# Kernel tuning notes

Measured on AMD Instinct MI355X. Metric: run time of the kernel, lower is better.

## Reference

```python
import jax, jax.numpy as jnp
import numpy as np

N_HEAD = 12
N_EMBD = 768


def setup_inputs() -> dict:
    key = jax.random.key(0)
    k1, k2, k3, k4, k5 = jax.random.split(key, 5)
    B, T, C = 4, 2048, N_EMBD
    s = 0.02
    x = jax.random.normal(k1, (B, T, C), dtype=jnp.float32)
    w_attn = jax.random.normal(k2, (C, 3 * C), dtype=jnp.float32) * s
    b_attn = jnp.zeros((3 * C,), dtype=jnp.float32)
    w_proj = jax.random.normal(k3, (C, C), dtype=jnp.float32) * s
    b_proj = jnp.zeros((C,), dtype=jnp.float32)
    return {"x": x, "w_attn": w_attn, "b_attn": b_attn, "w_proj": w_proj, "b_proj": b_proj}


def reference(x, w_attn, b_attn, w_proj, b_proj):
    # dropout omitted (eval mode / dropout=0.0)
    B, T, C = x.shape
    H = N_HEAD
    D = C // H  # head dim
    qkv = x @ w_attn + b_attn                      # [B,T,3C]
    q, k, v = jnp.split(qkv, 3, axis=-1)
    q = q.reshape(B, T, H, D).transpose(0, 2, 1, 3)  # [B,H,T,D]
    k = k.reshape(B, T, H, D).transpose(0, 2, 1, 3)
    v = v.reshape(B, T, H, D).transpose(0, 2, 1, 3)
    att = jnp.einsum('bhqd,bhkd->bhqk', q, k) * (1.0 / np.sqrt(D))  # [B,H,T,T]
    causal = jnp.tril(jnp.ones((T, T), dtype=bool))
    att = jnp.where(causal[None, None], att, -jnp.inf)
    att = jax.nn.softmax(att, axis=-1)
    y = jnp.einsum('bhqk,bhkd->bhqd', att, v)      # [B,H,T,D]
    y = y.transpose(0, 2, 1, 3).reshape(B, T, C)
    return y @ w_proj + b_proj
```

## Files before the change

kernel.cpp:

```cpp
#include <hip/hip_runtime.h>
#include <stdint.h>

typedef unsigned short ushort_t;

#define T_SEQ 2048
#define BATCH 4
#define NHEAD 12
#define CEMB 768
#define HDIM 64
#define C3 2304

__device__ __forceinline__ ushort_t f2b_hw(float f) {
  union { __bf16 h; ushort_t u; } p;
  p.h = (__bf16)f;
  return p.u;
}
__device__ __forceinline__ uint32_t pkbf16(float lo, float hi) {
  union { __bf16 h[2]; uint32_t u; } p;
  p.h[0] = (__bf16)lo; p.h[1] = (__bf16)hi;
  return p.u;
}

typedef __attribute__((address_space(3))) unsigned int lds_u32_t;
typedef const __attribute__((address_space(1))) unsigned int glb_u32_t;
__device__ __forceinline__ void async_cp16(const void* g, void* l) {
  __builtin_amdgcn_global_load_lds((glb_u32_t*)g, (lds_u32_t*)l, 16, 0, 0);
}

__global__ __launch_bounds__(256) void prep_k(const float* __restrict__ x, ushort_t* __restrict__ xb,
                                              const float* __restrict__ wa, ushort_t* __restrict__ wT,
                                              const float* __restrict__ wp, ushort_t* __restrict__ wpT) {
  const int blk = blockIdx.x;
  const int tid = threadIdx.x;
  if (blk < 3072) {
    const int i = blk * 256 + tid;
    float4 a = ((const float4*)x)[2 * i];
    float4 b = ((const float4*)x)[2 * i + 1];
    uint4 v;
    v.x = pkbf16(a.x, a.y); v.y = pkbf16(a.z, a.w);
    v.z = pkbf16(b.x, b.y); v.w = pkbf16(b.z, b.w);
    ((uint4*)xb)[i] = v;
    return;
  }
  __shared__ ushort_t tile[32][33];
  const float* in; ushort_t* out; int R, C, bx, by;
  if (blk < 4800) {
    const int t = blk - 3072;
    in = wa; out = wT; R = CEMB; C = C3;
    bx = t % 72; by = t / 72;
  } else {
    const int t = blk - 4800;
    in = wp; out = wpT; R = CEMB; C = CEMB;
    bx = t % 24; by = t / 24;
  }
  const int tx = tid & 31, ty = tid >> 5;
  const int c0 = bx * 32, r0 = by * 32;
  for (int i = ty; i < 32; i += 8)
    tile[i][tx] = f2b_hw(in[(size_t)(r0 + i) * C + c0 + tx]);
  __syncthreads();
  for (int i = ty; i < 32; i += 8)
    out[(size_t)(c0 + i) * R + r0 + tx] = tile[tx][i];
}

typedef __bf16 bf16x8 __attribute__((ext_vector_type(8)));
typedef float f32x4 __attribute__((ext_vector_type(4)));

template <bool OUTF, int BM>
__global__ __launch_bounds__(256) void gemm_bt(const ushort_t* __restrict__ A,
                                               const ushort_t* __restrict__ Bt,
                                               const float* __restrict__ bias,
                                               void* __restrict__ Cv,
                                               int M, int N, int K) {
  constexpr int TM = BM / 32;
  __shared__ ushort_t As[2 * BM * 32];
  __shared__ ushort_t Bs[2 * 128 * 32];
  const int tid = threadIdx.x;
  const int m0 = blockIdx.y * BM, n0 = blockIdx.x * 128;
  const int wid = tid >> 6, lane = tid & 63;
  const int quad = lane >> 4, l15 = lane & 15;
  const int wm = (wid >> 1) * (BM / 2), wn = (wid & 1) * 64;
  f32x4 acc[TM][4] = {};

  const int e0 = tid * 8;
  const int r0s = e0 >> 5, c0s = e0 & 31;
  const int e1 = e0 + 2048;
  const int r1s = e1 >> 5, c1s = e1 & 31;

  for (int k0 = 0; k0 < K; k0 += 64) {
    __syncthreads();
#pragma unroll
    for (int p = 0; p < 2; p++) {
      const int kc = k0 + p * 32;
      async_cp16(&A[(size_t)(m0 + r0s) * K + kc + c0s], &As[p * BM * 32 + e0]);
      if constexpr (BM == 128)
        async_cp16(&A[(size_t)(m0 + r1s) * K + kc + c1s], &As[p * BM * 32 + e1]);
      async_cp16(&Bt[(size_t)(n0 + r0s) * K + kc + c0s], &Bs[p * 128 * 32 + e0]);
      async_cp16(&Bt[(size_t)(n0 + r1s) * K + kc + c1s], &Bs[p * 128 * 32 + e1]);
    }
    __syncthreads();
    bf16x8 af[TM][2], bfr[4][2];
#pragma unroll
    for (int t = 0; t < TM; t++)
#pragma unroll
      for (int p = 0; p < 2; p++)
        af[t][p] = *(const bf16x8*)&As[p * BM * 32 + (wm + t * 16 + l15) * 32 + quad * 8];
#pragma unroll
    for (int t = 0; t < 4; t++)
#pragma unroll
      for (int p = 0; p < 2; p++)
        bfr[t][p] = *(const bf16x8*)&Bs[p * 128 * 32 + (wn + t * 16 + l15) * 32 + quad * 8];
#pragma unroll
    for (int p = 0; p < 2; p++)
#pragma unroll
      for (int tm = 0; tm < TM; tm++)
#pragma unroll
        for (int tn = 0; tn < 4; tn++)
          acc[tm][tn] = __builtin_amdgcn_mfma_f32_16x16x32_bf16(af[tm][p], bfr[tn][p], acc[tm][tn], 0, 0, 0);
  }

#pragma unroll
  for (int tm = 0; tm < TM; tm++) {
    const int row = m0 + wm + tm * 16 + quad * 4;
#pragma unroll
    for (int tn = 0; tn < 4; tn++) {
      const int col = n0 + wn + tn * 16 + l15;
      const float bv = bias[col];
#pragma unroll
      for (int rr = 0; rr < 4; rr++) {
        if constexpr (OUTF)
          ((float*)Cv)[(size_t)(row + rr) * N + col] = acc[tm][tn][rr] + bv;
        else
          ((ushort_t*)Cv)[(size_t)(row + rr) * N + col] = f2b_hw(acc[tm][tn][rr] + bv);
      }
    }
  }
}

#define PSTR 72

__device__ __forceinline__ void commit_v(ushort_t* __restrict__ vt, int vd0, int vpair,
                                         uint4 pV0, uint4 pV1) {
  union { uint32_t u[4]; uint4 v; } a, c;
  a.v = pV0; c.v = pV1;
#pragma unroll
  for (int j = 0; j < 8; j++) {
    uint32_t pk = __builtin_amdgcn_perm(c.u[j >> 1], a.u[j >> 1],
                                        (j & 1) ? 0x07060302u : 0x05040100u);
    *(uint32_t*)&vt[(vd0 + j) * PSTR + 2 * vpair] = pk;
  }
}

__global__ __launch_bounds__(256) void attn_mfma_k(const ushort_t* __restrict__ qkv,
                                                   ushort_t* __restrict__ y) {
  __shared__ ushort_t Ksm[2][2][64 * 32];
  __shared__ ushort_t Vt[2][64 * PSTR];
  __shared__ ushort_t Plds[4][16 * PSTR];

  const int jj = blockIdx.x;
  const int h = blockIdx.y, b = blockIdx.z;
  const int tid = threadIdx.x;
  const int w = tid >> 6, lane = tid & 63;
  const int quad = lane >> 4, l15 = lane & 15;

  const int e0 = tid * 8;
  const int vpair = tid & 31, vd0 = (tid >> 5) * 8;
  const ushort_t* kbase = qkv + ((size_t)(b * T_SEQ) + (e0 >> 5)) * C3 + CEMB + h * HDIM + (e0 & 31);
  const ushort_t* vbase = qkv + ((size_t)(b * T_SEQ) + 2 * vpair) * C3 + 2 * CEMB + h * HDIM + vd0;
  const size_t step = (size_t)64 * C3;

  int koff[4], voff[4];
#pragma unroll
  for (int m = 0; m < 4; m++) koff[m] = (m * 16 + l15) * 32 + quad * 8;
#pragma unroll
  for (int nd = 0; nd < 4; nd++) voff[nd] = (nd * 16 + l15) * PSTR + quad * 8;
  const int poffR = l15 * PSTR + quad * 8;
  const int poffW = l15 * PSTR + quad * 4;
  const int qloc = 16 * w + l15;

  const float C2 = 0.18033688011112042f;

  for (int ph = 0; ph < 2; ++ph) {
    const int qt = ph ? (31 - jj) : jj;
    const int nkt = qt + 1;
    const int qw = qt * 64 + w * 16;

    bf16x8 qB[2];
#pragma unroll
    for (int kb = 0; kb < 2; kb++)
      qB[kb] = *(const bf16x8*)&qkv[((size_t)(b * T_SEQ + qw + l15)) * C3 +
                                    h * HDIM + kb * 32 + quad * 8];

    f32x4 o2[4] = {};
    float m_i = -3e38f, l_i = 0.f;

    __syncthreads();

    const ushort_t* kp = kbase;
    const ushort_t* vp = vbase;
    uint4 pV0 = *(const uint4*)vp, pV1 = *(const uint4*)(vp + C3);
    async_cp16(kp, &Ksm[0][0][e0]);
    async_cp16(kp + 32, &Ksm[0][1][e0]);
    commit_v(Vt[0], vd0, vpair, pV0, pV1);
    vp += step;
    pV0 = *(const uint4*)vp; pV1 = *(const uint4*)(vp + C3);

    for (int kt = 0; kt < nkt; ++kt) {
      __syncthreads();
      if (kt + 1 < nkt) {
        const int nb = (kt + 1) & 1;
        kp += step;
        async_cp16(kp, &Ksm[nb][0][e0]);
        async_cp16(kp + 32, &Ksm[nb][1][e0]);
        commit_v(Vt[nb], vd0, vpair, pV0, pV1);
        if (kt + 2 < nkt) {
          vp += step;
          pV0 = *(const uint4*)vp; pV1 = *(const uint4*)(vp + C3);
        }
      }
      const int cb = kt & 1;

      bf16x8 kA[4][2];
#pragma unroll
      for (int m = 0; m < 4; m++) {
        kA[m][0] = *(const bf16x8*)&Ksm[cb][0][koff[m]];
        kA[m][1] = *(const bf16x8*)&Ksm[cb][1][koff[m]];
      }
      f32x4 st[4] = {};
#pragma unroll
      for (int m = 0; m < 4; m++) {
        st[m] = __builtin_amdgcn_mfma_f32_16x16x32_bf16(kA[m][0], qB[0], st[m], 0, 0, 0);
        st[m] = __builtin_amdgcn_mfma_f32_16x16x32_bf16(kA[m][1], qB[1], st[m], 0, 0, 0);
      }

      if (kt == qt) {
#pragma unroll
        for (int m = 0; m < 4; m++)
#pragma unroll
          for (int r = 0; r < 4; r++)
            if (m * 16 + quad * 4 + r > qloc) st[m][r] = -3e38f;
      }

      float mx = st[0][0];
#pragma unroll
      for (int m = 0; m < 4; m++)
#pragma unroll
        for (int r = 0; r < 4; r++) mx = fmaxf(mx, st[m][r]);
      mx = fmaxf(mx, __shfl_xor(mx, 16, 64));
      mx = fmaxf(mx, __shfl_xor(mx, 32, 64));
      const float mn = fmaxf(m_i, mx);
      const float al = exp2f((m_i - mn) * C2);
      m_i = mn;
      const float mnc = mn * C2;
      float ls = 0.f;
#pragma unroll
      for (int m = 0; m < 4; m++)
#pragma unroll
        for (int r = 0; r < 4; r++) {
          float p = exp2f(fmaf(st[m][r], C2, -mnc));
          st[m][r] = p;
          ls += p;
        }
      ls += __shfl_xor(ls, 16, 64);
      ls += __shfl_xor(ls, 32, 64);
      l_i = l_i * al + ls;

#pragma unroll
      for (int m = 0; m < 4; m++) {
        uint2 pk;
        pk.x = pkbf16(st[m][0], st[m][1]);
        pk.y = pkbf16(st[m][2], st[m][3]);
        *(uint2*)&Plds[w][poffW + m * 16] = pk;
      }
#pragma unroll
      for (int nd = 0; nd < 4; nd++)
#pragma unroll
        for (int r = 0; r < 4; r++) o2[nd][r] *= al;

      asm volatile("s_waitcnt lgkmcnt(0)" ::: "memory");

      bf16x8 ap[2], bv[4][2];
#pragma unroll
      for (int kb = 0; kb < 2; kb++)
        ap[kb] = *(const bf16x8*)&Plds[w][poffR + kb * 32];
#pragma unroll
      for (int nd = 0; nd < 4; nd++)
#pragma unroll
        for (int kb = 0; kb < 2; kb++)
          bv[nd][kb] = *(const bf16x8*)&Vt[cb][voff[nd] + kb * 32];
#pragma unroll
      for (int nd = 0; nd < 4; nd++) {
        o2[nd] = __builtin_amdgcn_mfma_f32_16x16x32_bf16(bv[nd][0], ap[0], o2[nd], 0, 0, 0);
        o2[nd] = __builtin_amdgcn_mfma_f32_16x16x32_bf16(bv[nd][1], ap[1], o2[nd], 0, 0, 0);
      }
    }

    {
      const float inv = 1.0f / l_i;
      const int qg = qw + l15;
      ushort_t* yp = y + ((size_t)(b * T_SEQ + qg)) * CEMB + h * HDIM + quad * 4;
#pragma unroll
      for (int nd = 0; nd < 4; nd++) {
        uint2 pk;
        pk.x = pkbf16(o2[nd][0] * inv, o2[nd][1] * inv);
        pk.y = pkbf16(o2[nd][2] * inv, o2[nd][3] * inv);
        *(uint2*)(yp + nd * 16) = pk;
      }
    }
  }
}

extern "C" void kernel_launch(void* const* d_in, const int* in_sizes, int n_in,
                              void* d_out, int out_size, void* d_ws, size_t ws_size,
                              hipStream_t stream) {
  const float* x      = (const float*)d_in[0];
  const float* w_attn = (const float*)d_in[1];
  const float* b_attn = (const float*)d_in[2];
  const float* w_proj = (const float*)d_in[3];
  const float* b_proj = (const float*)d_in[4];
  float* out = (float*)d_out;

  char* ws = (char*)d_ws;
  ushort_t* qkv = (ushort_t*)ws;
  ushort_t* y   = qkv + (size_t)8192 * 2304;
  ushort_t* xb  = y + (size_t)8192 * 768;
  ushort_t* wT  = xb + (size_t)8192 * 768;
  ushort_t* wpT = wT + (size_t)2304 * 768;

  prep_k<<<5376, 256, 0, stream>>>(x, xb, w_attn, wT, w_proj, wpT);

  gemm_bt<false, 128><<<dim3(C3 / 128, 8192 / 128), 256, 0, stream>>>(xb, wT, b_attn, qkv, 8192, C3, CEMB);

  attn_mfma_k<<<dim3(16, NHEAD, BATCH), 256, 0, stream>>>(qkv, y);

  gemm_bt<true, 64><<<dim3(CEMB / 128, 8192 / 64), 256, 0, stream>>>(y, wpT, b_proj, out, 8192, CEMB, CEMB);
}
```

Measured before the change: 233.3 us.

## Swizzle attention LDS layouts, one query tile per block, lazy softmax rescale

Replaces the padded LDS strides for V, P and K with XOR-swizzled unpadded layouts, so shared-memory bank conflicts drop and less LDS is used. The paired-tile scheme, where each block handled tile jj and tile 31-jj, becomes one query tile per block. The grid is 48x32 and the heaviest tiles are issued first. Online softmax now skips the running-max update and accumulator rescale when no new score exceeds the old max by more than a threshold, which saves shuffles and multiplies at some numerical risk. Load balance now depends on the hardware scheduler rather than on explicit pairing.

Result: no change. 231.1 us (-0.9%).

```diff
diff --git a/kernel.cpp b/kernel.cpp
--- a/kernel.cpp
+++ b/kernel.cpp
@@ -136,9 +136,9 @@
   }
 }
 
-#define PSTR 72
-
-__device__ __forceinline__ void commit_v(ushort_t* __restrict__ vt, int vd0, int vpair,
+#define VSTR 64
+
+__device__ __forceinline__ void commit_v(ushort_t* __restrict__ vt, const int* __restrict__ offs,
                                          uint4 pV0, uint4 pV1) {
   union { uint32_t u[4]; uint4 v; } a, c;
   a.v = pV0; c.v = pV1;
@@ -146,165 +146,176 @@
   for (int j = 0; j < 8; j++) {
     uint32_t pk = __builtin_amdgcn_perm(c.u[j >> 1], a.u[j >> 1],
                                         (j & 1) ? 0x07060302u : 0x05040100u);
-    *(uint32_t*)&vt[(vd0 + j) * PSTR + 2 * vpair] = pk;
+    *(uint32_t*)&vt[offs[j]] = pk;
   }
 }
 
 __global__ __launch_bounds__(256) void attn_mfma_k(const ushort_t* __restrict__ qkv,
                                                    ushort_t* __restrict__ y) {
   __shared__ ushort_t Ksm[2][2][64 * 32];
-  __shared__ ushort_t Vt[2][64 * PSTR];
-  __shared__ ushort_t Plds[4][16 * PSTR];
-
-  const int jj = blockIdx.x;
-  const int h = blockIdx.y, b = blockIdx.z;
+  __shared__ ushort_t Vt[2][64 * VSTR];
+  __shared__ ushort_t Plds[4][16 * VSTR];
+
+  const int qt = 31 - blockIdx.y;
+  const int h = blockIdx.x >> 2, b = blockIdx.x & 3;
   const int tid = threadIdx.x;
   const int w = tid >> 6, lane = tid & 63;
   const int quad = lane >> 4, l15 = lane & 15;
+  const int nkt = qt + 1;
+  const int qw = qt * 64 + w * 16;
 
   const int e0 = tid * 8;
+  const int kchunk = (tid & 3) ^ ((tid >> 3) & 3);
+  const ushort_t* kbase = qkv + ((size_t)(b * T_SEQ) + (tid >> 2)) * C3 + CEMB + h * HDIM + kchunk * 8;
   const int vpair = tid & 31, vd0 = (tid >> 5) * 8;
-  const ushort_t* kbase = qkv + ((size_t)(b * T_SEQ) + (e0 >> 5)) * C3 + CEMB + h * HDIM + (e0 & 31);
   const ushort_t* vbase = qkv + ((size_t)(b * T_SEQ) + 2 * vpair) * C3 + 2 * CEMB + h * HDIM + vd0;
   const size_t step = (size_t)64 * C3;
 
-  int koff[4], voff[4];
-#pragma unroll
-  for (int m = 0; m < 4; m++) koff[m] = (m * 16 + l15) * 32 + quad * 8;
-#pragma unroll
-  for (int nd = 0; nd < 4; nd++) voff[nd] = (nd * 16 + l15) * PSTR + quad * 8;
-  const int poffR = l15 * PSTR + quad * 8;
-  const int poffW = l15 * PSTR + quad * 4;
+  int voffw[8];
+#pragma unroll
+  for (int j = 0; j < 8; j++)
+    voffw[j] = (vd0 + j) * VSTR + (((vpair >> 2) ^ j) << 3) + ((vpair & 3) << 1);
+
+  const int sw7 = l15 & 7;
+  int koff[4];
+#pragma unroll
+  for (int m = 0; m < 4; m++)
+    koff[m] = (m * 16 + l15) * 32 + ((quad ^ ((l15 >> 1) & 3)) << 3);
+  int apoff[2];
+#pragma unroll
+  for (int kb = 0; kb < 2; kb++)
+    apoff[kb] = l15 * VSTR + (((quad + 4 * kb) ^ sw7) << 3);
+  int poffWm[4];
+#pragma unroll
+  for (int m = 0; m < 4; m++)
+    poffWm[m] = l15 * VSTR + (((2 * m + (quad >> 1)) ^ sw7) << 3) + ((quad & 1) << 2);
   const int qloc = 16 * w + l15;
 
   const float C2 = 0.18033688011112042f;
 
-  for (int ph = 0; ph < 2; ++ph) {
-    const int qt = ph ? (31 - jj) : jj;
-    const int nkt = qt + 1;
-    const int qw = qt * 64 + w * 16;
-
-    bf16x8 qB[2];
+  bf16x8 qB[2];
+#pragma unroll
+  for (int kb = 0; kb < 2; kb++)
+    qB[kb] = *(const bf16x8*)&qkv[((size_t)(b * T_SEQ + qw + l15)) * C3 +
+                                  h * HDIM + kb * 32 + quad * 8];
+
+  f32x4 o2[4] = {};
+  float m_i = -3e38f, l_i = 0.f;
+
+  const ushort_t* kp = kbase;
+  const ushort_t* vp = vbase;
+  uint4 pV0 = *(const uint4*)vp, pV1 = *(const uint4*)(vp + C3);
+  async_cp16(kp, &Ksm[0][0][e0]);
+  async_cp16(kp + 32, &Ksm[0][1][e0]);
+  commit_v(Vt[0], voffw, pV0, pV1);
+  vp += step;
+  pV0 = *(const uint4*)vp; pV1 = *(const uint4*)(vp + C3);
+
+  for (int kt = 0; kt < nkt; ++kt) {
+    __syncthreads();
+    if (kt + 1 < nkt) {
+      const int nb = (kt + 1) & 1;
+      kp += step;
+      async_cp16(kp, &Ksm[nb][0][e0]);
+      async_cp16(kp + 32, &Ksm[nb][1][e0]);
+      commit_v(Vt[nb], voffw, pV0, pV1);
+      if (kt + 2 < nkt) {
+        vp += step;
+        pV0 = *(const uint4*)vp; pV1 = *(const uint4*)(vp + C3);
+      }
+    }
+    const int cb = kt & 1;
+
+    bf16x8 kA[4][2];
+#pragma unroll
+    for (int m = 0; m < 4; m++) {
+      kA[m][0] = *(const bf16x8*)&Ksm[cb][0][koff[m]];
+      kA[m][1] = *(const bf16x8*)&Ksm[cb][1][koff[m]];
+    }
+    f32x4 st[4] = {};
+#pragma unroll
+    for (int m = 0; m < 4; m++) {
+      st[m] = __builtin_amdgcn_mfma_f32_16x16x32_bf16(kA[m][0], qB[0], st[m], 0, 0, 0);
+      st[m] = __builtin_amdgcn_mfma_f32_16x16x32_bf16(kA[m][1], qB[1], st[m], 0, 0, 0);
+    }
+
+    if (kt == qt) {
+#pragma unroll
+      for (int m = 0; m < 4; m++)
+#pragma unroll
+        for (int r = 0; r < 4; r++)
+          if (m * 16 + quad * 4 + r > qloc) st[m][r] = -3e38f;
+    }
+
+    f32x4 mq;
+#pragma unroll
+    for (int r = 0; r < 4; r++)
+      mq[r] = fmaxf(fmaxf(st[0][r], st[1][r]), fmaxf(st[2][r], st[3][r]));
+    const float mxl = fmaxf(fmaxf(mq[0], mq[1]), fmaxf(mq[2], mq[3]));
+
+    float al = 1.f;
+    if (!__all(mxl - m_i <= 22.18f)) {
+      float mx = fmaxf(mxl, __shfl_xor(mxl, 16, 64));
+      mx = fmaxf(mx, __shfl_xor(mx, 32, 64));
+      const float mnew = fmaxf(m_i, mx);
+      al = exp2f((m_i - mnew) * C2);
+      m_i = mnew;
+#pragma unroll
+      for (int nd = 0; nd < 4; nd++)
+#pragma unroll
+        for (int r = 0; r < 4; r++) o2[nd][r] *= al;
+    }
+    const float mnc = m_i * C2;
+#pragma unroll
+    for (int m = 0; m < 4; m++)
+#pragma unroll
+      for (int r = 0; r < 4; r++)
+        st[m][r] = exp2f(fmaf(st[m][r], C2, -mnc));
+    f32x4 s4;
+#pragma unroll
+    for (int r = 0; r < 4; r++)
+      s4[r] = (st[0][r] + st[1][r]) + (st[2][r] + st[3][r]);
+    float ls = (s4[0] + s4[1]) + (s4[2] + s4[3]);
+    ls += __shfl_xor(ls, 16, 64);
+    ls += __shfl_xor(ls, 32, 64);
+    l_i = l_i * al + ls;
+
+#pragma unroll
+    for (int m = 0; m < 4; m++) {
+      uint2 pk;
+      pk.x = pkbf16(st[m][0], st[m][1]);
+      pk.y = pkbf16(st[m][2], st[m][3]);
+      *(uint2*)&Plds[w][poffWm[m]] = pk;
+    }
+
+    asm volatile("s_waitcnt lgkmcnt(0)" ::: "memory");
+
+    bf16x8 ap[2], bv[4][2];
 #pragma unroll
     for (int kb = 0; kb < 2; kb++)
-      qB[kb] = *(const bf16x8*)&qkv[((size_t)(b * T_SEQ + qw + l15)) * C3 +
-                                    h * HDIM + kb * 32 + quad * 8];
-
-    f32x4 o2[4] = {};
-    float m_i = -3e38f, l_i = 0.f;
-
-    __syncthreads();
-
-    const ushort_t* kp = kbase;
-    const ushort_t* vp = vbase;
-    uint4 pV0 = *(const uint4*)vp, pV1 = *(const uint4*)(vp + C3);
-    async_cp16(kp, &Ksm[0][0][e0]);
-    async_cp16(kp + 32, &Ksm[0][1][e0]);
-    commit_v(Vt[0], vd0, vpair, pV0, pV1);
-    vp += step;
-    pV0 = *(const uint4*)vp; pV1 = *(const uint4*)(vp + C3);
-
-    for (int kt = 0; kt < nkt; ++kt) {
-      __syncthreads();
-      if (kt + 1 < nkt) {
-        const int nb = (kt + 1) & 1;
-        kp += step;
-        async_cp16(kp, &Ksm[nb][0][e0]);
-        async_cp16(kp + 32, &Ksm[nb][1][e0]);
-        commit_v(Vt[nb], vd0, vpair, pV0, pV1);
-        if (kt + 2 < nkt) {
-          vp += step;
-          pV0 = *(const uint4*)vp; pV1 = *(const uint4*)(vp + C3);
-        }
-      }
-      const int cb = kt & 1;
-
-      bf16x8 kA[4][2];
-#pragma unroll
-      for (int m = 0; m < 4; m++) {
-        kA[m][0] = *(const bf16x8*)&Ksm[cb][0][koff[m]];
-        kA[m][1] = *(const bf16x8*)&Ksm[cb][1][koff[m]];
-      }
-      f32x4 st[4] = {};
-#pragma unroll
-      for (int m = 0; m < 4; m++) {
-        st[m] = __builtin_amdgcn_mfma_f32_16x16x32_bf16(kA[m][0], qB[0], st[m], 0, 0, 0);
-        st[m] = __builtin_amdgcn_mfma_f32_16x16x32_bf16(kA[m][1], qB[1], st[m], 0, 0, 0);
-      }
-
-      if (kt == qt) {
-#pragma unroll
-        for (int m = 0; m < 4; m++)
-#pragma unroll
-          for (int r = 0; r < 4; r++)
-            if (m * 16 + quad * 4 + r > qloc) st[m][r] = -3e38f;
-      }
-
-      float mx = st[0][0];
-#pragma unroll
-      for (int m = 0; m < 4; m++)
-#pragma unroll
-        for (int r = 0; r < 4; r++) mx = fmaxf(mx, st[m][r]);
-      mx = fmaxf(mx, __shfl_xor(mx, 16, 64));
-      mx = fmaxf(mx, __shfl_xor(mx, 32, 64));
-      const float mn = fmaxf(m_i, mx);
-      const float al = exp2f((m_i - mn) * C2);
-      m_i = mn;
-      const float mnc = mn * C2;
-      float ls = 0.f;
-#pragma unroll
-      for (int m = 0; m < 4; m++)
-#pragma unroll
-        for (int r = 0; r < 4; r++) {
-          float p = exp2f(fmaf(st[m][r], C2, -mnc));
-          st[m][r] = p;
-          ls += p;
-        }
-      ls += __shfl_xor(ls, 16, 64);
-      ls += __shfl_xor(ls, 32, 64);
-      l_i = l_i * al + ls;
-
-#pragma unroll
-      for (int m = 0; m < 4; m++) {
-        uint2 pk;
-        pk.x = pkbf16(st[m][0], st[m][1]);
-        pk.y = pkbf16(st[m][2], st[m][3]);
-        *(uint2*)&Plds[w][poffW + m * 16] = pk;
-      }
-#pragma unroll
-      for (int nd = 0; nd < 4; nd++)
-#pragma unroll
-        for (int r = 0; r < 4; r++) o2[nd][r] *= al;
-
-      asm volatile("s_waitcnt lgkmcnt(0)" ::: "memory");
-
-      bf16x8 ap[2], bv[4][2];
+      ap[kb] = *(const bf16x8*)&Plds[w][apoff[kb]];
+#pragma unroll
+    for (int nd = 0; nd < 4; nd++)
 #pragma unroll
       for (int kb = 0; kb < 2; kb++)
-        ap[kb] = *(const bf16x8*)&Plds[w][poffR + kb * 32];
-#pragma unroll
-      for (int nd = 0; nd < 4; nd++)
-#pragma unroll
-        for (int kb = 0; kb < 2; kb++)
-          bv[nd][kb] = *(const bf16x8*)&Vt[cb][voff[nd] + kb * 32];
-#pragma unroll
-      for (int nd = 0; nd < 4; nd++) {
-        o2[nd] = __builtin_amdgcn_mfma_f32_16x16x32_bf16(bv[nd][0], ap[0], o2[nd], 0, 0, 0);
-        o2[nd] = __builtin_amdgcn_mfma_f32_16x16x32_bf16(bv[nd][1], ap[1], o2[nd], 0, 0, 0);
-      }
-    }
-
-    {
-      const float inv = 1.0f / l_i;
-      const int qg = qw + l15;
-      ushort_t* yp = y + ((size_t)(b * T_SEQ + qg)) * CEMB + h * HDIM + quad * 4;
-#pragma unroll
-      for (int nd = 0; nd < 4; nd++) {
-        uint2 pk;
-        pk.x = pkbf16(o2[nd][0] * inv, o2[nd][1] * inv);
-        pk.y = pkbf16(o2[nd][2] * inv, o2[nd][3] * inv);
-        *(uint2*)(yp + nd * 16) = pk;
-      }
+        bv[nd][kb] = *(const bf16x8*)&Vt[cb][nd * 1024 + apoff[kb]];
+#pragma unroll
+    for (int nd = 0; nd < 4; nd++) {
+      o2[nd] = __builtin_amdgcn_mfma_f32_16x16x32_bf16(bv[nd][0], ap[0], o2[nd], 0, 0, 0);
+      o2[nd] = __builtin_amdgcn_mfma_f32_16x16x32_bf16(bv[nd][1], ap[1], o2[nd], 0, 0, 0);
+    }
+  }
+
+  {
+    const float inv = 1.0f / l_i;
+    const int qg = qw + l15;
+    ushort_t* yp = y + ((size_t)(b * T_SEQ + qg)) * CEMB + h * HDIM + quad * 4;
+#pragma unroll
+    for (int nd = 0; nd < 4; nd++) {
+      uint2 pk;
+      pk.x = pkbf16(o2[nd][0] * inv, o2[nd][1] * inv);
+      pk.y = pkbf16(o2[nd][2] * inv, o2[nd][3] * inv);
+      *(uint2*)(yp + nd * 16) = pk;
     }
   }
 }
@@ -330,7 +341,7 @@
 
   gemm_bt<false, 128><<<dim3(C3 / 128, 8192 / 128), 256, 0, stream>>>(xb, wT, b_attn, qkv, 8192, C3, CEMB);
 
-  attn_mfma_k<<<dim3(16, NHEAD, BATCH), 256, 0, stream>>>(qkv, y);
+  attn_mfma_k<<<dim3(48, 32), 256, 0, stream>>>(qkv, y);
 
   gemm_bt<true, 64><<<dim3(CEMB / 128, 8192 / 64), 256, 0, stream>>>(y, wpT, b_proj, out, 8192, CEMB, CEMB);
 }
```
